# Kernel tuning notes

Hardware: AMD Instinct MI355X
Metric: run time of the kernel (lower is better)

The kernel has to match this reference:

```python
import jax, jax.numpy as jnp
import numpy as np

NUM_GRAPHS = 64
NEG_SLOPE = 0.2  # DGL GATConv default negative_slope


def _gat_layer(h, W, a_l, a_r, b, src, dst, n_nodes):
    # DGL GATConv, num_heads=1: feat = h @ W (no bias in fc),
    # e_ij = LeakyReLU(a_l . feat_src + a_r . feat_dst), softmax over incoming
    # edges of each dst node, out_dst = sum alpha * feat_src + bias.
    feat = h @ W                      # [N, D]
    el = feat @ a_l                   # [N]
    er = feat @ a_r                   # [N]
    e = jax.nn.leaky_relu(el[src] + er[dst], NEG_SLOPE)   # [E]
    m = jax.ops.segment_max(e, dst, num_segments=n_nodes)  # per-dst max
    ex = jnp.exp(e - m[dst])
    s = jax.ops.segment_sum(ex, dst, num_segments=n_nodes)
    alpha = ex / s[dst]               # edge softmax
    out = jax.ops.segment_sum(feat[src] * alpha[:, None], dst, num_segments=n_nodes)
    return out + b


def setup_inputs() -> dict:
    key = jax.random.key(0)
    ks = jax.random.split(key, 12)
    N, E, D_IN, D_H, C = 100000, 1600000, 128, 128, 2
    h = jax.random.normal(ks[0], (N, D_IN), dtype=jnp.float32)
    src = jax.random.randint(ks[1], (E,), 0, N)
    dst = jax.random.randint(ks[2], (E,), 0, N)
    graph_id = jnp.sort(jax.random.randint(ks[3], (N,), 0, NUM_GRAPHS))
    sc = 1.0 / np.sqrt(D_IN)
    params = {
        'W1': jax.random.normal(ks[4], (D_IN, D_H), dtype=jnp.float32) * sc,
        'al1': jax.random.normal(ks[5], (D_H,), dtype=jnp.float32) * sc,
        'ar1': jax.random.normal(ks[6], (D_H,), dtype=jnp.float32) * sc,
        'b1': jnp.zeros((D_H,), dtype=jnp.float32),
        'W2': jax.random.normal(ks[7], (D_H, D_H), dtype=jnp.float32) * sc,
        'al2': jax.random.normal(ks[8], (D_H,), dtype=jnp.float32) * sc,
        'ar2': jax.random.normal(ks[9], (D_H,), dtype=jnp.float32) * sc,
        'b2': jnp.zeros((D_H,), dtype=jnp.float32),
        'Wfc': jax.random.normal(ks[10], (D_H, C), dtype=jnp.float32) * sc,
        'bfc': jnp.zeros((C,), dtype=jnp.float32),
    }
    return dict(h=h, src=src, dst=dst, graph_id=graph_id, **params)


def reference(h, src, dst, graph_id, W1, al1, ar1, b1, W2, al2, ar2, b2, Wfc, bfc):
    n_nodes = h.shape[0]
    x = jax.nn.relu(_gat_layer(h, W1, al1, ar1, b1, src, dst, n_nodes))
    x = jax.nn.relu(_gat_layer(x, W2, al2, ar2, b2, src, dst, n_nodes))
    # dgl.mean_nodes over the batched graph
    counts = jax.ops.segment_sum(jnp.ones((n_nodes,), x.dtype), graph_id,
                                 num_segments=NUM_GRAPHS)
    hg = jax.ops.segment_sum(x, graph_id, num_segments=NUM_GRAPHS)
    hg = hg / jnp.clip(counts, 1.0)[:, None]          # [G, D]
    logits = hg @ Wfc + bfc                            # [G, C]
    return jax.nn.log_softmax(logits, axis=-1)
```

## Files before the change

kernel.cpp:

```cpp
#include <hip/hip_runtime.h>
#include <math.h>

#define NUM_GRAPHS 64
#define D 128
#define MT 64
#define ETILE 4096
#define PCH 16

typedef __attribute__((ext_vector_type(8))) short bf16x8;
typedef __attribute__((ext_vector_type(4))) float f32x4;
typedef __attribute__((ext_vector_type(2))) float f32x2;

__device__ __forceinline__ unsigned bf16rne(float x) {
    unsigned u = __float_as_uint(x);
    return (u + 0x7fffu + ((u >> 16) & 1u)) >> 16;
}
__device__ __forceinline__ float bflo(unsigned u) { return __uint_as_float(u << 16); }
__device__ __forceinline__ float bfhi(unsigned u) { return __uint_as_float(u & 0xffff0000u); }

__device__ __forceinline__ unsigned encf(float f) {
    unsigned u = __float_as_uint(f);
    return (u & 0x80000000u) ? ~u : (u | 0x80000000u);
}
__device__ __forceinline__ float decf(unsigned e) {
    unsigned u = (e & 0x80000000u) ? (e & 0x7fffffffu) : ~e;
    return __uint_as_float(u);
}


__global__ __launch_bounds__(256) void k_front(
    const int* __restrict__ dst, int* __restrict__ bhist, int E, int nbT,
    const float* __restrict__ W1, const float* __restrict__ W2,
    unsigned short* __restrict__ Wt1, unsigned short* __restrict__ Wt2,
    const int* __restrict__ gid, int* __restrict__ gs, int* __restrict__ ge, int N) {
    __shared__ int h[1024];
    int b = blockIdx.x;
    int tid = threadIdx.x;
    if (b < nbT) {
        for (int i = tid; i < 1024; i += 256) h[i] = 0;
        __syncthreads();
        int e0 = b * ETILE;
        int e1 = min(e0 + ETILE, E);
        for (int i = e0 + tid; i < e1; i += 256) atomicAdd(&h[dst[i] >> 7], 1);
        __syncthreads();
        for (int i = tid; i < 1024; i += 256)
            if (h[i]) atomicAdd(&bhist[i], h[i]);
    } else if (b < nbT + 16) {
        int bb = b - nbT;
        const float* W = (bb & 8) ? W2 : W1;
        unsigned short* Wt = (bb & 8) ? Wt2 : Wt1;
        int n = (bb & 7) * 16 + (tid >> 4);
        int c = tid & 15;
        unsigned v[8];
        #pragma unroll
        for (int j = 0; j < 8; ++j) v[j] = bf16rne(W[(c * 8 + j) * D + n]);
        uint4 pk;
        pk.x = v[0] | (v[1] << 16);
        pk.y = v[2] | (v[3] << 16);
        pk.z = v[4] | (v[5] << 16);
        pk.w = v[6] | (v[7] << 16);
        ((uint4*)Wt)[n * 16 + c] = pk;
    } else {
        int n = (b - nbT - 16) * 256 + tid;
        if (n >= N) return;
        int g = gid[n];
        if (n == 0 || gid[n - 1] != g) gs[g] = n + 1;
        if (n == N - 1 || gid[n + 1] != g) ge[g] = n + 1;
    }
}

__global__ __launch_bounds__(1024) void k_bucket_scan(const int* __restrict__ bhist,
                                                      int* __restrict__ bbase,
                                                      int* __restrict__ bcur,
                                                      int NB, int E,
                                                      int* __restrict__ row_ptr, int N) {
    __shared__ int sm[1024];
    int t = threadIdx.x;
    int v = (t < NB) ? bhist[t] : 0;
    sm[t] = v;
    __syncthreads();
    for (int off = 1; off < 1024; off <<= 1) {
        int y = (t >= off) ? sm[t - off] : 0;
        __syncthreads();
        sm[t] += y;
        __syncthreads();
    }
    if (t < NB) { bbase[t] = sm[t] - v; bcur[t] = sm[t] - v; }
    if (t == 0) { bbase[NB] = E; row_ptr[N] = E; }
}

__global__ __launch_bounds__(256) void k_partition(const int* __restrict__ src,
                                                   const int* __restrict__ dst,
                                                   int* __restrict__ bcur,
                                                   unsigned* __restrict__ part, int E) {
    __shared__ int h[1024];
    __shared__ int cur[1024];
    int tid = threadIdx.x;
    for (int i = tid; i < 1024; i += 256) h[i] = 0;
    __syncthreads();
    int e0 = blockIdx.x * ETILE;
    int e1 = min(e0 + ETILE, E);
    for (int i = e0 + tid; i < e1; i += 256) atomicAdd(&h[dst[i] >> 7], 1);
    __syncthreads();
    for (int i = tid; i < 1024; i += 256) {
        int c = h[i];
        cur[i] = c ? atomicAdd(&bcur[i], c) : 0;
    }
    __syncthreads();
    for (int i = e0 + tid; i < e1; i += 256) {
        int d = dst[i];
        int b = d >> 7;
        int pos = atomicAdd(&cur[b], 1);
        part[pos] = (unsigned)src[i] | ((unsigned)(d & 127) << 17);
    }
}


__global__ __launch_bounds__(256) void k_gemm_mfma_sort(
    const void* __restrict__ Xv, int x_fp32,
    const unsigned short* __restrict__ Wt16,
    const float* __restrict__ al, const float* __restrict__ ar,
    unsigned short* __restrict__ feat16, float* __restrict__ el,
    float* __restrict__ er, unsigned* __restrict__ glmax_u, int N, int gemmBlocks,
    const unsigned* __restrict__ part, const int* __restrict__ bbase,
    int* __restrict__ row_ptr, int* __restrict__ csr_src) {
    __shared__ uint4 WsU[128 * 16];
    __shared__ uint4 XsU[MT * 16];
    __shared__ float smax[4];
    int bx = blockIdx.x;
    int T = gridDim.x;
    int g0 = (int)((long long)bx * gemmBlocks / T);
    int g1 = (int)((long long)(bx + 1) * gemmBlocks / T);
    int tid = threadIdx.x;

    if (g1 == g0) {
        int b = bx - g0;
        int base = bbase[b];
        int bcnt = bbase[b + 1] - base;
        int* ldeg = (int*)XsU;
        int* lcur = ldeg + 128;
        if (tid < 128) ldeg[tid] = 0;
        __syncthreads();
        for (int i = tid; i < bcnt; i += 256)
            atomicAdd(&ldeg[part[base + i] >> 17], 1);
        __syncthreads();
        int myv = (tid < 128) ? ldeg[tid] : 0;
        for (int off = 1; off < 128; off <<= 1) {
            int y = 0;
            if (tid < 128 && tid >= off) y = ldeg[tid - off];
            __syncthreads();
            if (tid < 128) ldeg[tid] += y;
            __syncthreads();
        }
        if (tid < 128) {
            int excl = ldeg[tid] - myv;
            int node = (b << 7) + tid;
            if (node < N) row_ptr[node] = base + excl;
            lcur[tid] = base + excl;
        }
        __syncthreads();
        for (int i = tid; i < bcnt; i += 256) {
            unsigned v = part[base + i];
            int pos = atomicAdd(&lcur[v >> 17], 1);
            csr_src[pos] = (int)(v & 0x1FFFFu);
        }
        return;
    }

    int row0 = g0 * MT;

    for (int idx = tid; idx < 128 * 16; idx += 256) {
        int n = idx >> 4, c = idx & 15;
        WsU[(n << 4) | (c ^ (n & 15))] = ((const uint4*)Wt16)[idx];
    }
    if (x_fp32) {
        const float4* X4 = (const float4*)Xv;
        for (int idx = tid; idx < MT * 16; idx += 256) {
            int n = idx >> 4, c = idx & 15;
            int row = row0 + n;
            uint4 o = make_uint4(0, 0, 0, 0);
            if (row < N) {
                float4 f0 = X4[(size_t)row * 32 + c * 2];
                float4 f1 = X4[(size_t)row * 32 + c * 2 + 1];
                o.x = bf16rne(f0.x) | (bf16rne(f0.y) << 16);
                o.y = bf16rne(f0.z) | (bf16rne(f0.w) << 16);
                o.z = bf16rne(f1.x) | (bf16rne(f1.y) << 16);
                o.w = bf16rne(f1.z) | (bf16rne(f1.w) << 16);
            }
            XsU[(n << 4) | (c ^ (n & 15))] = o;
        }
    } else {
        const uint4* X16 = (const uint4*)Xv;
        for (int idx = tid; idx < MT * 16; idx += 256) {
            int n = idx >> 4, c = idx & 15;
            int row = row0 + n;
            uint4 o = make_uint4(0, 0, 0, 0);
            if (row < N) o = X16[(size_t)row * 16 + c];
            XsU[(n << 4) | (c ^ (n & 15))] = o;
        }
    }
    __syncthreads();

    int lane = tid & 63, w = tid >> 6;
    int quad = lane >> 4, l16 = lane & 15;
    const bf16x8* WsF = (const bf16x8*)WsU;
    const bf16x8* XsF = (const bf16x8*)XsU;
    f32x4 acc[8];
    #pragma unroll
    for (int i = 0; i < 8; ++i) acc[i] = (f32x4){0.f, 0.f, 0.f, 0.f};

    int arow = w * 16 + l16;
    #pragma unroll
    for (int ks = 0; ks < 4; ++ks) {
        int c = ks * 4 + quad;
        bf16x8 A = XsF[(arow << 4) | (c ^ l16)];
        #pragma unroll
        for (int nt = 0; nt < 8; ++nt) {
            bf16x8 B = WsF[((nt * 16 + l16) << 4) | (c ^ l16)];
            acc[nt] = __builtin_amdgcn_mfma_f32_16x16x32_bf16(A, B, acc[nt], 0, 0, 0);
        }
    }

    float alv[8], arv[8];
    #pragma unroll
    for (int nt = 0; nt < 8; ++nt) { alv[nt] = al[nt * 16 + l16]; arv[nt] = ar[nt * 16 + l16]; }
    float lmax = -1e30f;
    #pragma unroll
    for (int r = 0; r < 4; ++r) {
        float pl = 0.f, pr = 0.f;
        #pragma unroll
        for (int nt = 0; nt < 8; ++nt) { pl += acc[nt][r] * alv[nt]; pr += acc[nt][r] * arv[nt]; }
        #pragma unroll
        for (int o = 1; o < 16; o <<= 1) { pl += __shfl_xor(pl, o); pr += __shfl_xor(pr, o); }
        int row = row0 + w * 16 + quad * 4 + r;
        if (l16 == 0 && row < N) { el[row] = pl; er[row] = pr; }
        lmax = fmaxf(lmax, pl);
    }
    lmax = fmaxf(lmax, __shfl_xor(lmax, 16));
    lmax = fmaxf(lmax, __shfl_xor(lmax, 32));
    if (lane == 0) smax[w] = lmax;

    unsigned short* XsS = (unsigned short*)XsU;
    #pragma unroll
    for (int nt = 0; nt < 8; ++nt)
        #pragma unroll
        for (int r = 0; r < 4; ++r) {
            int lrow = w * 16 + quad * 4 + r;
            int col = nt * 16 + l16;
            int ch = col >> 3;
            int sc = ch ^ (lrow & 15);
            XsS[lrow * 128 + sc * 8 + (col & 7)] = (unsigned short)bf16rne(acc[nt][r]);
        }
    __syncthreads();
    if (tid == 0) {
        float bm = fmaxf(fmaxf(smax[0], smax[1]), fmaxf(smax[2], smax[3]));
        atomicMax(glmax_u, encf(bm));
    }
    for (int idx = tid; idx < MT * 16; idx += 256) {
        int n = idx >> 4, c = idx & 15;
        int row = row0 + n;
        if (row < N) ((uint4*)feat16)[(size_t)row * 16 + c] = XsU[(n << 4) | (c ^ (n & 15))];
    }
}


__global__ __launch_bounds__(256) void k_aggregate(
    const unsigned short* __restrict__ feat16, const float* __restrict__ el,
    const float* __restrict__ er, const int* __restrict__ row_ptr,
    const int* __restrict__ csr_src, const float* __restrict__ bias,
    const unsigned* __restrict__ glmax_u, unsigned short* __restrict__ outv,
    const int* __restrict__ gid, int dopool, float* __restrict__ hgpart,
    int* __restrict__ gtag, float* __restrict__ hg_extra, int N) {
    __shared__ float bacc[4][16][8];
    __shared__ int gsm[4];
    int tid = threadIdx.x;
    int wv = tid >> 6;
    int lane = tid & 63;
    int wid = blockIdx.x * 4 + wv;
    bool act = wid < N;

    int beg = 0, end = 0;
    float erd = 0.f;
    if (act) { beg = row_ptr[wid]; end = row_ptr[wid + 1]; erd = er[wid]; }
    float M = decf(glmax_u[0]) + erd;
    M = fmaxf(M, 0.2f * M);

    int qa = lane >> 4, sub = lane & 15;
    const char* fb = (const char*)feat16 + (sub << 4);
    f32x2 a0 = {0.f, 0.f}, a1 = {0.f, 0.f}, a2 = {0.f, 0.f}, a3 = {0.f, 0.f};
    float s = 0.f;
    int j = beg + qa;
    for (; j + 12 < end; j += 16) {
        int sn0 = csr_src[j], sn1 = csr_src[j + 4];
        int sn2 = csr_src[j + 8], sn3 = csr_src[j + 12];
        float t0 = el[sn0] + erd, t1 = el[sn1] + erd;
        float t2 = el[sn2] + erd, t3 = el[sn3] + erd;
        uint4 q0 = *(const uint4*)(fb + ((unsigned)sn0 << 8));
        uint4 q1 = *(const uint4*)(fb + ((unsigned)sn1 << 8));
        uint4 q2 = *(const uint4*)(fb + ((unsigned)sn2 << 8));
        uint4 q3 = *(const uint4*)(fb + ((unsigned)sn3 << 8));
        t0 = fmaxf(t0, 0.2f * t0); t1 = fmaxf(t1, 0.2f * t1);
        t2 = fmaxf(t2, 0.2f * t2); t3 = fmaxf(t3, 0.2f * t3);
        float w0 = __expf(t0 - M), w1 = __expf(t1 - M);
        float w2 = __expf(t2 - M), w3 = __expf(t3 - M);
        s += (w0 + w1) + (w2 + w3);
        f32x2 f;
        f.x = bflo(q0.x); f.y = bfhi(q0.x); a0 += w0 * f;
        f.x = bflo(q0.y); f.y = bfhi(q0.y); a1 += w0 * f;
        f.x = bflo(q0.z); f.y = bfhi(q0.z); a2 += w0 * f;
        f.x = bflo(q0.w); f.y = bfhi(q0.w); a3 += w0 * f;
        f.x = bflo(q1.x); f.y = bfhi(q1.x); a0 += w1 * f;
        f.x = bflo(q1.y); f.y = bfhi(q1.y); a1 += w1 * f;
        f.x = bflo(q1.z); f.y = bfhi(q1.z); a2 += w1 * f;
        f.x = bflo(q1.w); f.y = bfhi(q1.w); a3 += w1 * f;
        f.x = bflo(q2.x); f.y = bfhi(q2.x); a0 += w2 * f;
        f.x = bflo(q2.y); f.y = bfhi(q2.y); a1 += w2 * f;
        f.x = bflo(q2.z); f.y = bfhi(q2.z); a2 += w2 * f;
        f.x = bflo(q2.w); f.y = bfhi(q2.w); a3 += w2 * f;
        f.x = bflo(q3.x); f.y = bfhi(q3.x); a0 += w3 * f;
        f.x = bflo(q3.y); f.y = bfhi(q3.y); a1 += w3 * f;
        f.x = bflo(q3.z); f.y = bfhi(q3.z); a2 += w3 * f;
        f.x = bflo(q3.w); f.y = bfhi(q3.w); a3 += w3 * f;
    }
    for (; j + 4 < end; j += 8) {
        int sn0 = csr_src[j], sn1 = csr_src[j + 4];
        float t0 = el[sn0] + erd, t1 = el[sn1] + erd;
        uint4 q0 = *(const uint4*)(fb + ((unsigned)sn0 << 8));
        uint4 q1 = *(const uint4*)(fb + ((unsigned)sn1 << 8));
        t0 = fmaxf(t0, 0.2f * t0); t1 = fmaxf(t1, 0.2f * t1);
        float w0 = __expf(t0 - M), w1 = __expf(t1 - M);
        s += w0 + w1;
        f32x2 f;
        f.x = bflo(q0.x); f.y = bfhi(q0.x); a0 += w0 * f;
        f.x = bflo(q0.y); f.y = bfhi(q0.y); a1 += w0 * f;
        f.x = bflo(q0.z); f.y = bfhi(q0.z); a2 += w0 * f;
        f.x = bflo(q0.w); f.y = bfhi(q0.w); a3 += w0 * f;
        f.x = bflo(q1.x); f.y = bfhi(q1.x); a0 += w1 * f;
        f.x = bflo(q1.y); f.y = bfhi(q1.y); a1 += w1 * f;
        f.x = bflo(q1.z); f.y = bfhi(q1.z); a2 += w1 * f;
        f.x = bflo(q1.w); f.y = bfhi(q1.w); a3 += w1 * f;
    }
    if (j < end) {
        int sn = csr_src[j];
        float t = el[sn] + erd;
        uint4 q = *(const uint4*)(fb + ((unsigned)sn << 8));
        t = fmaxf(t, 0.2f * t);
        float w = __expf(t - M);
        s += w;
        f32x2 f;
        f.x = bflo(q.x); f.y = bfhi(q.x); a0 += w * f;
        f.x = bflo(q.y); f.y = bfhi(q.y); a1 += w * f;
        f.x = bflo(q.z); f.y = bfhi(q.z); a2 += w * f;
        f.x = bflo(q.w); f.y = bfhi(q.w); a3 += w * f;
    }
    float vr[8] = {a0.x, a0.y, a1.x, a1.y, a2.x, a2.y, a3.x, a3.y};
    #pragma unroll
    for (int c = 0; c < 8; ++c) {
        vr[c] += __shfl_xor(vr[c], 16);
        vr[c] += __shfl_xor(vr[c], 32);
    }
    s += __shfl_xor(s, 16);
    s += __shfl_xor(s, 32);
    float inv = (end > beg) ? 1.f / s : 0.f;

    if (dopool) {
        if (lane < 16) {
            float4 b0 = ((const float4*)bias)[lane * 2];
            float4 b1 = ((const float4*)bias)[lane * 2 + 1];
            float* bw = bacc[wv][lane];
            bw[0] = fmaxf(vr[0] * inv + b0.x, 0.f);
            bw[1] = fmaxf(vr[1] * inv + b0.y, 0.f);
            bw[2] = fmaxf(vr[2] * inv + b0.z, 0.f);
            bw[3] = fmaxf(vr[3] * inv + b0.w, 0.f);
            bw[4] = fmaxf(vr[4] * inv + b1.x, 0.f);
            bw[5] = fmaxf(vr[5] * inv + b1.y, 0.f);
            bw[6] = fmaxf(vr[6] * inv + b1.z, 0.f);
            bw[7] = fmaxf(vr[7] * inv + b1.w, 0.f);
        }
        if (lane == 0) gsm[wv] = act ? gid[wid] : -1;
        __syncthreads();
        int g0 = gsm[0];
        bool uni = (gsm[1] == g0) && (gsm[2] == g0) && (gsm[3] == g0) && (g0 >= 0);
        if (tid < 128) {
            int sb = tid >> 3, k = tid & 7;
            if (uni) {
                float sum = bacc[0][sb][k] + bacc[1][sb][k] + bacc[2][sb][k] + bacc[3][sb][k];
                hgpart[(size_t)blockIdx.x * D + tid] = sum;
            } else {
                #pragma unroll
                for (int u = 0; u < 4; ++u) {
                    int g = gsm[u];
                    if (g >= 0) atomicAdd(&hg_extra[g * D + tid], bacc[u][sb][k]);
                }
            }
        }
        if (tid == 0) gtag[blockIdx.x] = uni ? g0 : -1;
    } else if (act && lane < 16) {
        float4 b0 = ((const float4*)bias)[lane * 2];
        float4 b1 = ((const float4*)bias)[lane * 2 + 1];
        float v[8];
        v[0] = fmaxf(vr[0] * inv + b0.x, 0.f);
        v[1] = fmaxf(vr[1] * inv + b0.y, 0.f);
        v[2] = fmaxf(vr[2] * inv + b0.z, 0.f);
        v[3] = fmaxf(vr[3] * inv + b0.w, 0.f);
        v[4] = fmaxf(vr[4] * inv + b1.x, 0.f);
        v[5] = fmaxf(vr[5] * inv + b1.y, 0.f);
        v[6] = fmaxf(vr[6] * inv + b1.z, 0.f);
        v[7] = fmaxf(vr[7] * inv + b1.w, 0.f);
        uint4 pk;
        pk.x = bf16rne(v[0]) | (bf16rne(v[1]) << 16);
        pk.y = bf16rne(v[2]) | (bf16rne(v[3]) << 16);
        pk.z = bf16rne(v[4]) | (bf16rne(v[5]) << 16);
        pk.w = bf16rne(v[6]) | (bf16rne(v[7]) << 16);
        ((uint4*)outv)[(size_t)wid * 16 + lane] = pk;
    }
}


__global__ __launch_bounds__(128) void k_poolreduce(
    const float* __restrict__ hgpart, const int* __restrict__ gtag,
    const int* __restrict__ gs, const int* __restrict__ ge,
    float* __restrict__ hg_extra) {
    int g = blockIdx.x;
    int d = threadIdx.x;
    int s = gs[g] - 1, e = ge[g] - 1;
    if (s < 0 || e < s) return;
    int b0 = s >> 2, b1 = e >> 2;
    float acc = 0.f;
    for (int b = b0 + (int)blockIdx.y; b <= b1; b += PCH) {
        int t = gtag[b];
        float v = hgpart[(size_t)b * D + d];
        acc += (t == g) ? v : 0.f;
    }
    if (acc != 0.f) atomicAdd(&hg_extra[g * D + d], acc);
}


__global__ void k_final(const float* __restrict__ hg, const int* __restrict__ gs,
                        const int* __restrict__ ge, const float* __restrict__ Wfc,
                        const float* __restrict__ bfc, float* __restrict__ out) {
    int g = threadIdx.x;
    if (g >= NUM_GRAPHS) return;
    int start = gs[g] - 1, last = ge[g] - 1;
    float cnt = (start >= 0 && start <= last) ? (float)(last - start + 1) : 1.f;
    float ic = 1.f / cnt;
    float l0 = bfc[0], l1 = bfc[1];
    for (int d = 0; d < D; d++) {
        float v = hg[g * D + d] * ic;
        l0 += v * Wfc[2 * d];
        l1 += v * Wfc[2 * d + 1];
    }
    float mm = fmaxf(l0, l1);
    float lse = mm + logf(expf(l0 - mm) + expf(l1 - mm));
    out[2 * g] = l0 - lse;
    out[2 * g + 1] = l1 - lse;
}


extern "C" void kernel_launch(void* const* d_in, const int* in_sizes, int n_in,
                              void* d_out, int out_size, void* d_ws, size_t ws_size,
                              hipStream_t stream) {
    const float* h   = (const float*)d_in[0];
    const int* src   = (const int*)d_in[1];
    const int* dst   = (const int*)d_in[2];
    const int* gid   = (const int*)d_in[3];
    const float* W1  = (const float*)d_in[4];
    const float* al1 = (const float*)d_in[5];
    const float* ar1 = (const float*)d_in[6];
    const float* b1  = (const float*)d_in[7];
    const float* W2  = (const float*)d_in[8];
    const float* al2 = (const float*)d_in[9];
    const float* ar2 = (const float*)d_in[10];
    const float* b2  = (const float*)d_in[11];
    const float* Wfc = (const float*)d_in[12];
    const float* bfc = (const float*)d_in[13];
    float* out = (float*)d_out;

    int N = in_sizes[0] / D;
    int E = in_sizes[1];
    int NB = (N + 127) >> 7;
    int nbW = (N * 64 + 255) / 256;

    char* p = (char*)d_ws;
    unsigned short* feat16  = (unsigned short*)p; p += (size_t)N * D * 2;
    unsigned short* featAgg = (unsigned short*)p; p += (size_t)N * D * 2;
    float* el    = (float*)p; p += (size_t)N * 4;
    float* er    = (float*)p; p += (size_t)N * 4;
    int* row_ptr = (int*)p;   p += (size_t)(N + 4) * 4;
    int* csr_src = (int*)p;   p += (size_t)E * 4;
    size_t partBytes = (size_t)E * 4;
    size_t hgpBytes  = (size_t)nbW * D * 4;
    unsigned* part = (unsigned*)p;
    float* hgpart  = (float*)p;
    p += (partBytes > hgpBytes) ? partBytes : hgpBytes;
    int* bhist   = (int*)p;   p += 1028 * 4;
    unsigned* glmaxu = (unsigned*)p; p += 4 * 4;
    float* hg_extra = (float*)p; p += NUM_GRAPHS * D * 4;
    int* gs      = (int*)p;   p += NUM_GRAPHS * 4;
    int* ge      = (int*)p;   p += NUM_GRAPHS * 4;
    size_t zbytes = (char*)p - (char*)bhist;
    int* bbase   = (int*)p;   p += 1028 * 4;
    int* bcur    = (int*)p;   p += 1028 * 4;
    int* gtag    = (int*)p;   p += (size_t)nbW * 4;
    unsigned short* Wt1 = (unsigned short*)p; p += D * D * 2;
    unsigned short* Wt2 = (unsigned short*)p; p += D * D * 2;

    int nbN = (N + 255) / 256;
    int nbT = (E + ETILE - 1) / ETILE;
    int gemmB = (N + MT - 1) / MT;

    hipMemsetAsync(bhist, 0, zbytes, stream);

    k_front<<<nbT + 16 + nbN, 256, 0, stream>>>(dst, bhist, E, nbT,
                                                W1, W2, Wt1, Wt2, gid, gs, ge, N);
    k_bucket_scan<<<1, 1024, 0, stream>>>(bhist, bbase, bcur, NB, E, row_ptr, N);
    k_partition<<<nbT, 256, 0, stream>>>(src, dst, bcur, part, E);

    k_gemm_mfma_sort<<<gemmB + NB, 256, 0, stream>>>(
        h, 1, Wt1, al1, ar1, feat16, el, er, glmaxu, N, gemmB,
        part, bbase, row_ptr, csr_src);
    k_aggregate<<<nbW, 256, 0, stream>>>(feat16, el, er, row_ptr, csr_src,
                                         b1, glmaxu, featAgg, gid, 0,
                                         hgpart, gtag, hg_extra, N);

    k_gemm_mfma_sort<<<gemmB, 256, 0, stream>>>(
        featAgg, 0, Wt2, al2, ar2, feat16, el, er, glmaxu + 1, N, gemmB,
        part, bbase, row_ptr, csr_src);
    k_aggregate<<<nbW, 256, 0, stream>>>(feat16, el, er, row_ptr, csr_src,
                                         b2, glmaxu + 1, nullptr, gid, 1,
                                         hgpart, gtag, hg_extra, N);

    k_poolreduce<<<dim3(NUM_GRAPHS, PCH), 128, 0, stream>>>(hgpart, gtag, gs, ge,
                                                            hg_extra);
    k_final<<<1, 64, 0, stream>>>(hg_extra, gs, ge, Wfc, bfc, out);
}
```

Measured before the change: 358.3 us.

## Build CSR via per-node degree counts and global atomic scatter

Replaces the two-level bucket partition (a partition kernel plus an in-bucket local sort) with per-node degree counting in the front kernel, a per-bucket row_ptr scan kernel, and a direct scatter of src into CSR positions using global atomics on per-node cursors. This removes the intermediate part array and one full pass over the edges. In exchange it adds 1.6M global atomics on degree counts and 1.6M more on cursors, scattered across 100k nodes, and csr_src order within a row is no longer deterministic.

New measurement: 449.9 us. 1.26x slower.

```diff
diff --git a/kernel.cpp b/kernel.cpp
--- a/kernel.cpp
+++ b/kernel.cpp
@@ -29,7 +29,8 @@
 
 
 __global__ __launch_bounds__(256) void k_front(
-    const int* __restrict__ dst, int* __restrict__ bhist, int E, int nbT,
+    const int* __restrict__ dst, int* __restrict__ bhist, int* __restrict__ deg,
+    int E, int nbT,
     const float* __restrict__ W1, const float* __restrict__ W2,
     unsigned short* __restrict__ Wt1, unsigned short* __restrict__ Wt2,
     const int* __restrict__ gid, int* __restrict__ gs, int* __restrict__ ge, int N) {
@@ -41,7 +42,11 @@
         __syncthreads();
         int e0 = b * ETILE;
         int e1 = min(e0 + ETILE, E);
-        for (int i = e0 + tid; i < e1; i += 256) atomicAdd(&h[dst[i] >> 7], 1);
+        for (int i = e0 + tid; i < e1; i += 256) {
+            int d = dst[i];
+            atomicAdd(&h[d >> 7], 1);
+            atomicAdd(&deg[d], 1);
+        }
         __syncthreads();
         for (int i = tid; i < 1024; i += 256)
             if (h[i]) atomicAdd(&bhist[i], h[i]);
@@ -71,7 +76,6 @@
 
 __global__ __launch_bounds__(1024) void k_bucket_scan(const int* __restrict__ bhist,
                                                       int* __restrict__ bbase,
-                                                      int* __restrict__ bcur,
                                                       int NB, int E,
                                                       int* __restrict__ row_ptr, int N) {
     __shared__ int sm[1024];
@@ -85,33 +89,31 @@
         sm[t] += y;
         __syncthreads();
     }
-    if (t < NB) { bbase[t] = sm[t] - v; bcur[t] = sm[t] - v; }
+    if (t < NB) bbase[t] = sm[t] - v;
     if (t == 0) { bbase[NB] = E; row_ptr[N] = E; }
 }
 
-__global__ __launch_bounds__(256) void k_partition(const int* __restrict__ src,
-                                                   const int* __restrict__ dst,
-                                                   int* __restrict__ bcur,
-                                                   unsigned* __restrict__ part, int E) {
-    __shared__ int h[1024];
-    __shared__ int cur[1024];
-    int tid = threadIdx.x;
-    for (int i = tid; i < 1024; i += 256) h[i] = 0;
+
+__global__ __launch_bounds__(128) void k_rowptr(const int* __restrict__ deg,
+                                                const int* __restrict__ bbase,
+                                                int* __restrict__ row_ptr,
+                                                int* __restrict__ cur, int N) {
+    __shared__ int sm[128];
+    int b = blockIdx.x, t = threadIdx.x;
+    int node = (b << 7) + t;
+    int d = (node < N) ? deg[node] : 0;
+    sm[t] = d;
     __syncthreads();
-    int e0 = blockIdx.x * ETILE;
-    int e1 = min(e0 + ETILE, E);
-    for (int i = e0 + tid; i < e1; i += 256) atomicAdd(&h[dst[i] >> 7], 1);
-    __syncthreads();
-    for (int i = tid; i < 1024; i += 256) {
-        int c = h[i];
-        cur[i] = c ? atomicAdd(&bcur[i], c) : 0;
-    }
-    __syncthreads();
-    for (int i = e0 + tid; i < e1; i += 256) {
-        int d = dst[i];
-        int b = d >> 7;
-        int pos = atomicAdd(&cur[b], 1);
-        part[pos] = (unsigned)src[i] | ((unsigned)(d & 127) << 17);
+    for (int off = 1; off < 128; off <<= 1) {
+        int y = (t >= off) ? sm[t - off] : 0;
+        __syncthreads();
+        sm[t] += y;
+        __syncthreads();
+    }
+    if (node < N) {
+        int rp = bbase[b] + sm[t] - d;
+        row_ptr[node] = rp;
+        cur[node] = rp;
     }
 }
 
@@ -122,8 +124,8 @@
     const float* __restrict__ al, const float* __restrict__ ar,
     unsigned short* __restrict__ feat16, float* __restrict__ el,
     float* __restrict__ er, unsigned* __restrict__ glmax_u, int N, int gemmBlocks,
-    const unsigned* __restrict__ part, const int* __restrict__ bbase,
-    int* __restrict__ row_ptr, int* __restrict__ csr_src) {
+    const int* __restrict__ src, const int* __restrict__ dst,
+    int* __restrict__ cur, int* __restrict__ csr_src, int E) {
     __shared__ uint4 WsU[128 * 16];
     __shared__ uint4 XsU[MT * 16];
     __shared__ float smax[4];
@@ -134,35 +136,13 @@
     int tid = threadIdx.x;
 
     if (g1 == g0) {
-        int b = bx - g0;
-        int base = bbase[b];
-        int bcnt = bbase[b + 1] - base;
-        int* ldeg = (int*)XsU;
-        int* lcur = ldeg + 128;
-        if (tid < 128) ldeg[tid] = 0;
-        __syncthreads();
-        for (int i = tid; i < bcnt; i += 256)
-            atomicAdd(&ldeg[part[base + i] >> 17], 1);
-        __syncthreads();
-        int myv = (tid < 128) ? ldeg[tid] : 0;
-        for (int off = 1; off < 128; off <<= 1) {
-            int y = 0;
-            if (tid < 128 && tid >= off) y = ldeg[tid - off];
-            __syncthreads();
-            if (tid < 128) ldeg[tid] += y;
-            __syncthreads();
-        }
-        if (tid < 128) {
-            int excl = ldeg[tid] - myv;
-            int node = (b << 7) + tid;
-            if (node < N) row_ptr[node] = base + excl;
-            lcur[tid] = base + excl;
-        }
-        __syncthreads();
-        for (int i = tid; i < bcnt; i += 256) {
-            unsigned v = part[base + i];
-            int pos = atomicAdd(&lcur[v >> 17], 1);
-            csr_src[pos] = (int)(v & 0x1FFFFu);
+        int tile = bx - g0;
+        int e0 = tile * ETILE;
+        int e1 = min(e0 + ETILE, E);
+        for (int i = e0 + tid; i < e1; i += 256) {
+            int dnode = dst[i];
+            int pos = atomicAdd(&cur[dnode], 1);
+            csr_src[pos] = src[i];
         }
         return;
     }
@@ -487,20 +467,17 @@
     float* el    = (float*)p; p += (size_t)N * 4;
     float* er    = (float*)p; p += (size_t)N * 4;
     int* row_ptr = (int*)p;   p += (size_t)(N + 4) * 4;
+    int* cur     = (int*)p;   p += (size_t)(N + 4) * 4;
     int* csr_src = (int*)p;   p += (size_t)E * 4;
-    size_t partBytes = (size_t)E * 4;
-    size_t hgpBytes  = (size_t)nbW * D * 4;
-    unsigned* part = (unsigned*)p;
-    float* hgpart  = (float*)p;
-    p += (partBytes > hgpBytes) ? partBytes : hgpBytes;
+    float* hgpart = (float*)p; p += (size_t)nbW * D * 4;
     int* bhist   = (int*)p;   p += 1028 * 4;
+    int* deg     = (int*)p;   p += (size_t)(N + 4) * 4;
     unsigned* glmaxu = (unsigned*)p; p += 4 * 4;
     float* hg_extra = (float*)p; p += NUM_GRAPHS * D * 4;
     int* gs      = (int*)p;   p += NUM_GRAPHS * 4;
     int* ge      = (int*)p;   p += NUM_GRAPHS * 4;
     size_t zbytes = (char*)p - (char*)bhist;
     int* bbase   = (int*)p;   p += 1028 * 4;
-    int* bcur    = (int*)p;   p += 1028 * 4;
     int* gtag    = (int*)p;   p += (size_t)nbW * 4;
     unsigned short* Wt1 = (unsigned short*)p; p += D * D * 2;
     unsigned short* Wt2 = (unsigned short*)p; p += D * D * 2;
@@ -511,21 +488,21 @@
 
     hipMemsetAsync(bhist, 0, zbytes, stream);
 
-    k_front<<<nbT + 16 + nbN, 256, 0, stream>>>(dst, bhist, E, nbT,
+    k_front<<<nbT + 16 + nbN, 256, 0, stream>>>(dst, bhist, deg, E, nbT,
                                                 W1, W2, Wt1, Wt2, gid, gs, ge, N);
-    k_bucket_scan<<<1, 1024, 0, stream>>>(bhist, bbase, bcur, NB, E, row_ptr, N);
-    k_partition<<<nbT, 256, 0, stream>>>(src, dst, bcur, part, E);
-
-    k_gemm_mfma_sort<<<gemmB + NB, 256, 0, stream>>>(
+    k_bucket_scan<<<1, 1024, 0, stream>>>(bhist, bbase, NB, E, row_ptr, N);
+    k_rowptr<<<NB, 128, 0, stream>>>(deg, bbase, row_ptr, cur, N);
+
+    k_gemm_mfma_sort<<<gemmB + nbT, 256, 0, stream>>>(
         h, 1, Wt1, al1, ar1, feat16, el, er, glmaxu, N, gemmB,
-        part, bbase, row_ptr, csr_src);
+        src, dst, cur, csr_src, E);
     k_aggregate<<<nbW, 256, 0, stream>>>(feat16, el, er, row_ptr, csr_src,
                                          b1, glmaxu, featAgg, gid, 0,
                                          hgpart, gtag, hg_extra, N);
 
     k_gemm_mfma_sort<<<gemmB, 256, 0, stream>>>(
         featAgg, 0, Wt2, al2, ar2, feat16, el, er, glmaxu + 1, N, gemmB,
-        part, bbase, row_ptr, csr_src);
+        src, dst, cur, csr_src, E);
     k_aggregate<<<nbW, 256, 0, stream>>>(feat16, el, er, row_ptr, csr_src,
                                          b2, glmaxu + 1, nullptr, gid, 1,
                                          hgpart, gtag, hg_extra, N);
```

## Process two destination nodes per wavefront in GAT aggregation

Applied to the files above, without the earlier changes.

Each 64-lane wavefront now aggregates two destination nodes at once, with interleaved gather loops for the two nodes and separate tails for each. The goal is more independent memory loads in flight per wave and half as many blocks, which hides gather latency and reduces per-node launch and reduction overhead. The pooling partials, the tag layout and the poolreduce block indexing are changed to 8 nodes per block. The main loop now unrolls 2 edges per node instead of 4, and the two nodes may differ in degree, which leaves tail work serialized.

New measurement: 366.0 us. +2.2%, slower.

```diff
diff --git a/kernel.cpp b/kernel.cpp
--- a/kernel.cpp
+++ b/kernel.cpp
@@ -264,6 +264,12 @@
 }
 
 
+#define EFMA(q, wt, x0, x1, x2, x3) { f32x2 f; \
+    f.x = bflo((q).x); f.y = bfhi((q).x); x0 += (wt) * f; \
+    f.x = bflo((q).y); f.y = bfhi((q).y); x1 += (wt) * f; \
+    f.x = bflo((q).z); f.y = bfhi((q).z); x2 += (wt) * f; \
+    f.x = bflo((q).w); f.y = bfhi((q).w); x3 += (wt) * f; }
+
 __global__ __launch_bounds__(256) void k_aggregate(
     const unsigned short* __restrict__ feat16, const float* __restrict__ el,
     const float* __restrict__ er, const int* __restrict__ row_ptr,
@@ -271,148 +277,195 @@
     const unsigned* __restrict__ glmax_u, unsigned short* __restrict__ outv,
     const int* __restrict__ gid, int dopool, float* __restrict__ hgpart,
     int* __restrict__ gtag, float* __restrict__ hg_extra, int N) {
-    __shared__ float bacc[4][16][8];
-    __shared__ int gsm[4];
+    __shared__ float bacc[8][16][8];
+    __shared__ int gsm[8];
     int tid = threadIdx.x;
     int wv = tid >> 6;
     int lane = tid & 63;
-    int wid = blockIdx.x * 4 + wv;
-    bool act = wid < N;
-
-    int beg = 0, end = 0;
-    float erd = 0.f;
-    if (act) { beg = row_ptr[wid]; end = row_ptr[wid + 1]; erd = er[wid]; }
-    float M = decf(glmax_u[0]) + erd;
-    M = fmaxf(M, 0.2f * M);
+    int widA = blockIdx.x * 8 + wv * 2;
+    int widB = widA + 1;
+    bool actA = widA < N, actB = widB < N;
+
+    int begA = 0, endA = 0, begB = 0, endB = 0;
+    float erdA = 0.f, erdB = 0.f;
+    if (actA) { begA = row_ptr[widA]; endA = row_ptr[widA + 1]; erdA = er[widA]; }
+    if (actB) { begB = row_ptr[widB]; endB = row_ptr[widB + 1]; erdB = er[widB]; }
+    float gm = decf(glmax_u[0]);
+    float MA = gm + erdA; MA = fmaxf(MA, 0.2f * MA);
+    float MB = gm + erdB; MB = fmaxf(MB, 0.2f * MB);
 
     int qa = lane >> 4, sub = lane & 15;
     const char* fb = (const char*)feat16 + (sub << 4);
-    f32x2 a0 = {0.f, 0.f}, a1 = {0.f, 0.f}, a2 = {0.f, 0.f}, a3 = {0.f, 0.f};
-    float s = 0.f;
-    int j = beg + qa;
-    for (; j + 12 < end; j += 16) {
-        int sn0 = csr_src[j], sn1 = csr_src[j + 4];
-        int sn2 = csr_src[j + 8], sn3 = csr_src[j + 12];
-        float t0 = el[sn0] + erd, t1 = el[sn1] + erd;
-        float t2 = el[sn2] + erd, t3 = el[sn3] + erd;
-        uint4 q0 = *(const uint4*)(fb + ((unsigned)sn0 << 8));
-        uint4 q1 = *(const uint4*)(fb + ((unsigned)sn1 << 8));
-        uint4 q2 = *(const uint4*)(fb + ((unsigned)sn2 << 8));
-        uint4 q3 = *(const uint4*)(fb + ((unsigned)sn3 << 8));
-        t0 = fmaxf(t0, 0.2f * t0); t1 = fmaxf(t1, 0.2f * t1);
-        t2 = fmaxf(t2, 0.2f * t2); t3 = fmaxf(t3, 0.2f * t3);
-        float w0 = __expf(t0 - M), w1 = __expf(t1 - M);
-        float w2 = __expf(t2 - M), w3 = __expf(t3 - M);
-        s += (w0 + w1) + (w2 + w3);
-        f32x2 f;
-        f.x = bflo(q0.x); f.y = bfhi(q0.x); a0 += w0 * f;
-        f.x = bflo(q0.y); f.y = bfhi(q0.y); a1 += w0 * f;
-        f.x = bflo(q0.z); f.y = bfhi(q0.z); a2 += w0 * f;
-        f.x = bflo(q0.w); f.y = bfhi(q0.w); a3 += w0 * f;
-        f.x = bflo(q1.x); f.y = bfhi(q1.x); a0 += w1 * f;
-        f.x = bflo(q1.y); f.y = bfhi(q1.y); a1 += w1 * f;
-        f.x = bflo(q1.z); f.y = bfhi(q1.z); a2 += w1 * f;
-        f.x = bflo(q1.w); f.y = bfhi(q1.w); a3 += w1 * f;
-        f.x = bflo(q2.x); f.y = bfhi(q2.x); a0 += w2 * f;
-        f.x = bflo(q2.y); f.y = bfhi(q2.y); a1 += w2 * f;
-        f.x = bflo(q2.z); f.y = bfhi(q2.z); a2 += w2 * f;
-        f.x = bflo(q2.w); f.y = bfhi(q2.w); a3 += w2 * f;
-        f.x = bflo(q3.x); f.y = bfhi(q3.x); a0 += w3 * f;
-        f.x = bflo(q3.y); f.y = bfhi(q3.y); a1 += w3 * f;
-        f.x = bflo(q3.z); f.y = bfhi(q3.z); a2 += w3 * f;
-        f.x = bflo(q3.w); f.y = bfhi(q3.w); a3 += w3 * f;
-    }
-    for (; j + 4 < end; j += 8) {
-        int sn0 = csr_src[j], sn1 = csr_src[j + 4];
-        float t0 = el[sn0] + erd, t1 = el[sn1] + erd;
-        uint4 q0 = *(const uint4*)(fb + ((unsigned)sn0 << 8));
-        uint4 q1 = *(const uint4*)(fb + ((unsigned)sn1 << 8));
-        t0 = fmaxf(t0, 0.2f * t0); t1 = fmaxf(t1, 0.2f * t1);
-        float w0 = __expf(t0 - M), w1 = __expf(t1 - M);
-        s += w0 + w1;
-        f32x2 f;
-        f.x = bflo(q0.x); f.y = bfhi(q0.x); a0 += w0 * f;
-        f.x = bflo(q0.y); f.y = bfhi(q0.y); a1 += w0 * f;
-        f.x = bflo(q0.z); f.y = bfhi(q0.z); a2 += w0 * f;
-        f.x = bflo(q0.w); f.y = bfhi(q0.w); a3 += w0 * f;
-        f.x = bflo(q1.x); f.y = bfhi(q1.x); a0 += w1 * f;
-        f.x = bflo(q1.y); f.y = bfhi(q1.y); a1 += w1 * f;
-        f.x = bflo(q1.z); f.y = bfhi(q1.z); a2 += w1 * f;
-        f.x = bflo(q1.w); f.y = bfhi(q1.w); a3 += w1 * f;
-    }
-    if (j < end) {
-        int sn = csr_src[j];
-        float t = el[sn] + erd;
-        uint4 q = *(const uint4*)(fb + ((unsigned)sn << 8));
-        t = fmaxf(t, 0.2f * t);
-        float w = __expf(t - M);
-        s += w;
-        f32x2 f;
-        f.x = bflo(q.x); f.y = bfhi(q.x); a0 += w * f;
-        f.x = bflo(q.y); f.y = bfhi(q.y); a1 += w * f;
-        f.x = bflo(q.z); f.y = bfhi(q.z); a2 += w * f;
-        f.x = bflo(q.w); f.y = bfhi(q.w); a3 += w * f;
-    }
-    float vr[8] = {a0.x, a0.y, a1.x, a1.y, a2.x, a2.y, a3.x, a3.y};
+    f32x2 aA0 = {0.f,0.f}, aA1 = {0.f,0.f}, aA2 = {0.f,0.f}, aA3 = {0.f,0.f};
+    f32x2 aB0 = {0.f,0.f}, aB1 = {0.f,0.f}, aB2 = {0.f,0.f}, aB3 = {0.f,0.f};
+    float sA = 0.f, sB = 0.f;
+    int jA = begA + qa, jB = begB + qa;
+
+    for (; jA + 4 < endA && jB + 4 < endB; jA += 8, jB += 8) {
+        int na0 = csr_src[jA], na1 = csr_src[jA + 4];
+        int nb0 = csr_src[jB], nb1 = csr_src[jB + 4];
+        float ta0 = el[na0] + erdA, ta1 = el[na1] + erdA;
+        float tb0 = el[nb0] + erdB, tb1 = el[nb1] + erdB;
+        uint4 ua0 = *(const uint4*)(fb + ((unsigned)na0 << 8));
+        uint4 ua1 = *(const uint4*)(fb + ((unsigned)na1 << 8));
+        uint4 ub0 = *(const uint4*)(fb + ((unsigned)nb0 << 8));
+        uint4 ub1 = *(const uint4*)(fb + ((unsigned)nb1 << 8));
+        ta0 = fmaxf(ta0, 0.2f * ta0); ta1 = fmaxf(ta1, 0.2f * ta1);
+        tb0 = fmaxf(tb0, 0.2f * tb0); tb1 = fmaxf(tb1, 0.2f * tb1);
+        float wa0 = __expf(ta0 - MA), wa1 = __expf(ta1 - MA);
+        float wb0 = __expf(tb0 - MB), wb1 = __expf(tb1 - MB);
+        sA += wa0 + wa1; sB += wb0 + wb1;
+        EFMA(ua0, wa0, aA0, aA1, aA2, aA3)
+        EFMA(ua1, wa1, aA0, aA1, aA2, aA3)
+        EFMA(ub0, wb0, aB0, aB1, aB2, aB3)
+        EFMA(ub1, wb1, aB0, aB1, aB2, aB3)
+    }
+    for (; jA + 4 < endA; jA += 8) {
+        int na0 = csr_src[jA], na1 = csr_src[jA + 4];
+        float ta0 = el[na0] + erdA, ta1 = el[na1] + erdA;
+        uint4 ua0 = *(const uint4*)(fb + ((unsigned)na0 << 8));
+        uint4 ua1 = *(const uint4*)(fb + ((unsigned)na1 << 8));
+        ta0 = fmaxf(ta0, 0.2f * ta0); ta1 = fmaxf(ta1, 0.2f * ta1);
+        float wa0 = __expf(ta0 - MA), wa1 = __expf(ta1 - MA);
+        sA += wa0 + wa1;
+        EFMA(ua0, wa0, aA0, aA1, aA2, aA3)
+        EFMA(ua1, wa1, aA0, aA1, aA2, aA3)
+    }
+    if (jA < endA) {
+        int na0 = csr_src[jA];
+        float ta0 = el[na0] + erdA;
+        uint4 ua0 = *(const uint4*)(fb + ((unsigned)na0 << 8));
+        ta0 = fmaxf(ta0, 0.2f * ta0);
+        float wa0 = __expf(ta0 - MA);
+        sA += wa0;
+        EFMA(ua0, wa0, aA0, aA1, aA2, aA3)
+    }
+    for (; jB + 4 < endB; jB += 8) {
+        int nb0 = csr_src[jB], nb1 = csr_src[jB + 4];
+        float tb0 = el[nb0] + erdB, tb1 = el[nb1] + erdB;
+        uint4 ub0 = *(const uint4*)(fb + ((unsigned)nb0 << 8));
+        uint4 ub1 = *(const uint4*)(fb + ((unsigned)nb1 << 8));
+        tb0 = fmaxf(tb0, 0.2f * tb0); tb1 = fmaxf(tb1, 0.2f * tb1);
+        float wb0 = __expf(tb0 - MB), wb1 = __expf(tb1 - MB);
+        sB += wb0 + wb1;
+        EFMA(ub0, wb0, aB0, aB1, aB2, aB3)
+        EFMA(ub1, wb1, aB0, aB1, aB2, aB3)
+    }
+    if (jB < endB) {
+        int nb0 = csr_src[jB];
+        float tb0 = el[nb0] + erdB;
+        uint4 ub0 = *(const uint4*)(fb + ((unsigned)nb0 << 8));
+        tb0 = fmaxf(tb0, 0.2f * tb0);
+        float wb0 = __expf(tb0 - MB);
+        sB += wb0;
+        EFMA(ub0, wb0, aB0, aB1, aB2, aB3)
+    }
+
+    float vrA[8] = {aA0.x, aA0.y, aA1.x, aA1.y, aA2.x, aA2.y, aA3.x, aA3.y};
+    float vrB[8] = {aB0.x, aB0.y, aB1.x, aB1.y, aB2.x, aB2.y, aB3.x, aB3.y};
     #pragma unroll
     for (int c = 0; c < 8; ++c) {
-        vr[c] += __shfl_xor(vr[c], 16);
-        vr[c] += __shfl_xor(vr[c], 32);
-    }
-    s += __shfl_xor(s, 16);
-    s += __shfl_xor(s, 32);
-    float inv = (end > beg) ? 1.f / s : 0.f;
+        vrA[c] += __shfl_xor(vrA[c], 16);
+        vrA[c] += __shfl_xor(vrA[c], 32);
+        vrB[c] += __shfl_xor(vrB[c], 16);
+        vrB[c] += __shfl_xor(vrB[c], 32);
+    }
+    sA += __shfl_xor(sA, 16); sA += __shfl_xor(sA, 32);
+    sB += __shfl_xor(sB, 16); sB += __shfl_xor(sB, 32);
+    float invA = (endA > begA) ? 1.f / sA : 0.f;
+    float invB = (endB > begB) ? 1.f / sB : 0.f;
 
     if (dopool) {
         if (lane < 16) {
             float4 b0 = ((const float4*)bias)[lane * 2];
             float4 b1 = ((const float4*)bias)[lane * 2 + 1];
-            float* bw = bacc[wv][lane];
-            bw[0] = fmaxf(vr[0] * inv + b0.x, 0.f);
-            bw[1] = fmaxf(vr[1] * inv + b0.y, 0.f);
-            bw[2] = fmaxf(vr[2] * inv + b0.z, 0.f);
-            bw[3] = fmaxf(vr[3] * inv + b0.w, 0.f);
-            bw[4] = fmaxf(vr[4] * inv + b1.x, 0.f);
-            bw[5] = fmaxf(vr[5] * inv + b1.y, 0.f);
-            bw[6] = fmaxf(vr[6] * inv + b1.z, 0.f);
-            bw[7] = fmaxf(vr[7] * inv + b1.w, 0.f);
-        }
-        if (lane == 0) gsm[wv] = act ? gid[wid] : -1;
+            float* bw = bacc[wv * 2][lane];
+            bw[0] = fmaxf(vrA[0] * invA + b0.x, 0.f);
+            bw[1] = fmaxf(vrA[1] * invA + b0.y, 0.f);
+            bw[2] = fmaxf(vrA[2] * invA + b0.z, 0.f);
+            bw[3] = fmaxf(vrA[3] * invA + b0.w, 0.f);
+            bw[4] = fmaxf(vrA[4] * invA + b1.x, 0.f);
+            bw[5] = fmaxf(vrA[5] * invA + b1.y, 0.f);
+            bw[6] = fmaxf(vrA[6] * invA + b1.z, 0.f);
+            bw[7] = fmaxf(vrA[7] * invA + b1.w, 0.f);
+        } else if (lane < 32) {
+            int sb = lane - 16;
+            float4 b0 = ((const float4*)bias)[sb * 2];
+            float4 b1 = ((const float4*)bias)[sb * 2 + 1];
+            float* bw = bacc[wv * 2 + 1][sb];
+            bw[0] = fmaxf(vrB[0] * invB + b0.x, 0.f);
+            bw[1] = fmaxf(vrB[1] * invB + b0.y, 0.f);
+            bw[2] = fmaxf(vrB[2] * invB + b0.z, 0.f);
+            bw[3] = fmaxf(vrB[3] * invB + b0.w, 0.f);
+            bw[4] = fmaxf(vrB[4] * invB + b1.x, 0.f);
+            bw[5] = fmaxf(vrB[5] * invB + b1.y, 0.f);
+            bw[6] = fmaxf(vrB[6] * invB + b1.z, 0.f);
+            bw[7] = fmaxf(vrB[7] * invB + b1.w, 0.f);
+        }
+        if (lane == 0) {
+            gsm[wv * 2]     = actA ? gid[widA] : -1;
+            gsm[wv * 2 + 1] = actB ? gid[widB] : -1;
+        }
         __syncthreads();
         int g0 = gsm[0];
-        bool uni = (gsm[1] == g0) && (gsm[2] == g0) && (gsm[3] == g0) && (g0 >= 0);
+        bool uni = (g0 >= 0);
+        #pragma unroll
+        for (int u = 1; u < 8; ++u) uni = uni && (gsm[u] == g0);
         if (tid < 128) {
             int sb = tid >> 3, k = tid & 7;
             if (uni) {
-                float sum = bacc[0][sb][k] + bacc[1][sb][k] + bacc[2][sb][k] + bacc[3][sb][k];
+                float sum = 0.f;
+                #pragma unroll
+                for (int u = 0; u < 8; ++u) sum += bacc[u][sb][k];
                 hgpart[(size_t)blockIdx.x * D + tid] = sum;
             } else {
                 #pragma unroll
-                for (int u = 0; u < 4; ++u) {
+                for (int u = 0; u < 8; ++u) {
                     int g = gsm[u];
                     if (g >= 0) atomicAdd(&hg_extra[g * D + tid], bacc[u][sb][k]);
                 }
             }
         }
         if (tid == 0) gtag[blockIdx.x] = uni ? g0 : -1;
-    } else if (act && lane < 16) {
-        float4 b0 = ((const float4*)bias)[lane * 2];
-        float4 b1 = ((const float4*)bias)[lane * 2 + 1];
-        float v[8];
-        v[0] = fmaxf(vr[0] * inv + b0.x, 0.f);
-        v[1] = fmaxf(vr[1] * inv + b0.y, 0.f);
-        v[2] = fmaxf(vr[2] * inv + b0.z, 0.f);
-        v[3] = fmaxf(vr[3] * inv + b0.w, 0.f);
-        v[4] = fmaxf(vr[4] * inv + b1.x, 0.f);
-        v[5] = fmaxf(vr[5] * inv + b1.y, 0.f);
-        v[6] = fmaxf(vr[6] * inv + b1.z, 0.f);
-        v[7] = fmaxf(vr[7] * inv + b1.w, 0.f);
-        uint4 pk;
-        pk.x = bf16rne(v[0]) | (bf16rne(v[1]) << 16);
-        pk.y = bf16rne(v[2]) | (bf16rne(v[3]) << 16);
-        pk.z = bf16rne(v[4]) | (bf16rne(v[5]) << 16);
-        pk.w = bf16rne(v[6]) | (bf16rne(v[7]) << 16);
-        ((uint4*)outv)[(size_t)wid * 16 + lane] = pk;
+    } else {
+        if (actA && lane < 16) {
+            float4 b0 = ((const float4*)bias)[lane * 2];
+            float4 b1 = ((const float4*)bias)[lane * 2 + 1];
+            float v[8];
+            v[0] = fmaxf(vrA[0] * invA + b0.x, 0.f);
+            v[1] = fmaxf(vrA[1] * invA + b0.y, 0.f);
+            v[2] = fmaxf(vrA[2] * invA + b0.z, 0.f);
+            v[3] = fmaxf(vrA[3] * invA + b0.w, 0.f);
+            v[4] = fmaxf(vrA[4] * invA + b1.x, 0.f);
+            v[5] = fmaxf(vrA[5] * invA + b1.y, 0.f);
+            v[6] = fmaxf(vrA[6] * invA + b1.z, 0.f);
+            v[7] = fmaxf(vrA[7] * invA + b1.w, 0.f);
+            uint4 pk;
+            pk.x = bf16rne(v[0]) | (bf16rne(v[1]) << 16);
+            pk.y = bf16rne(v[2]) | (bf16rne(v[3]) << 16);
+            pk.z = bf16rne(v[4]) | (bf16rne(v[5]) << 16);
+            pk.w = bf16rne(v[6]) | (bf16rne(v[7]) << 16);
+            ((uint4*)outv)[(size_t)widA * 16 + lane] = pk;
+        } else if (actB && lane >= 16 && lane < 32) {
+            int sb = lane - 16;
+            float4 b0 = ((const float4*)bias)[sb * 2];
+            float4 b1 = ((const float4*)bias)[sb * 2 + 1];
+            float v[8];
+            v[0] = fmaxf(vrB[0] * invB + b0.x, 0.f);
+            v[1] = fmaxf(vrB[1] * invB + b0.y, 0.f);
+            v[2] = fmaxf(vrB[2] * invB + b0.z, 0.f);
+            v[3] = fmaxf(vrB[3] * invB + b0.w, 0.f);
+            v[4] = fmaxf(vrB[4] * invB + b1.x, 0.f);
+            v[5] = fmaxf(vrB[5] * invB + b1.y, 0.f);
+            v[6] = fmaxf(vrB[6] * invB + b1.z, 0.f);
+            v[7] = fmaxf(vrB[7] * invB + b1.w, 0.f);
+            uint4 pk;
+            pk.x = bf16rne(v[0]) | (bf16rne(v[1]) << 16);
+            pk.y = bf16rne(v[2]) | (bf16rne(v[3]) << 16);
+            pk.z = bf16rne(v[4]) | (bf16rne(v[5]) << 16);
+            pk.w = bf16rne(v[6]) | (bf16rne(v[7]) << 16);
+            ((uint4*)outv)[(size_t)widB * 16 + sb] = pk;
+        }
     }
 }
 
@@ -425,7 +478,7 @@
     int d = threadIdx.x;
     int s = gs[g] - 1, e = ge[g] - 1;
     if (s < 0 || e < s) return;
-    int b0 = s >> 2, b1 = e >> 2;
+    int b0 = s >> 3, b1 = e >> 3;
     float acc = 0.f;
     for (int b = b0 + (int)blockIdx.y; b <= b1; b += PCH) {
         int t = gtag[b];
@@ -479,7 +532,7 @@
     int N = in_sizes[0] / D;
     int E = in_sizes[1];
     int NB = (N + 127) >> 7;
-    int nbW = (N * 64 + 255) / 256;
+    int nbW = (N + 7) / 8;
 
     char* p = (char*)d_ws;
     unsigned short* feat16  = (unsigned short*)p; p += (size_t)N * D * 2;
```
